# Kernel optimization log

Measured on AMD Instinct MI355X. Metric: run time of the kernel, lower is better.

The kernel has to match this reference:

```python
import jax, jax.numpy as jnp
import numpy as np

NUM_HEADS = 4
LN_EPS = 1e-5
ALPHA_SCALE = 2.0


def setup_inputs() -> dict:
    key = jax.random.key(0)
    ks = jax.random.split(key, 8)
    bs, C, H, W = 64, 256, 56, 56
    T, D = 6, 192
    HW = H * W
    w = lambda k, shape: (jax.random.normal(k, shape, jnp.float32) * 0.02)
    return {
        "features": jax.random.normal(ks[0], (bs, C, H, W), jnp.float32),
        "tokens": jax.random.normal(ks[1], (T, bs, D), jnp.float32),
        # mlp: Linear(HW -> T)
        "mlp_w": w(ks[2], (T, HW)), "mlp_b": jnp.zeros((T,), jnp.float32),
        # q: Linear(D -> C)
        "q_w": w(ks[3], (C, D)), "q_b": jnp.zeros((C,), jnp.float32),
        # alpha: Linear(D -> C)
        "alpha_w": w(ks[4], (C, D)), "alpha_b": jnp.zeros((C,), jnp.float32),
        # proj: Linear(C -> D)
        "proj_w": w(ks[5], (D, C)), "proj_b": jnp.zeros((D,), jnp.float32),
        "ln_g": jnp.ones((D,), jnp.float32), "ln_b": jnp.zeros((D,), jnp.float32),
    }


def reference(features, tokens, mlp_w, mlp_b, q_w, q_b,
              alpha_w, alpha_b, proj_w, proj_b, ln_g, ln_b):
    bs, C, H, W = features.shape
    T, _, D = tokens.shape
    h = NUM_HEADS
    dh = C // h
    HW = H * W
    scale = dh ** -0.5

    f = features.reshape(bs, C, HW)

    # mlp branch: Linear over HW -> [bs, C, T] -> permute to [T, bs, C]
    t_sum = jnp.einsum('bcn,tn->tbc', f, mlp_w) + mlp_b[:, None, None]

    # attn branch: few tokens attend over H*W feature map (k reused as v)
    q = jnp.einsum('tbd,cd->tbc', tokens, q_w) + q_b          # [T, bs, C]
    q = q.reshape(T, bs, h, dh).transpose(1, 2, 0, 3)         # [bs, h, T, dh]
    k = f.reshape(bs, h, dh, HW)                              # [bs, h, dh, HW]
    attn = jnp.einsum('bhtd,bhdn->bhtn', q, k) * scale        # [bs, h, T, HW]
    a = jax.nn.softmax(attn, axis=-1)
    attn_out = jnp.einsum('bhtn,bhdn->bhtd', a, k)            # [bs, h, T, dh]
    t_a = attn_out.transpose(2, 0, 1, 3).reshape(T, bs, C)
    t_sum = t_sum + t_a

    # dynamic gate: h_sigmoid(alpha(tokens)) * 2.0
    alp = jnp.clip(jnp.einsum('tbd,cd->tbc', tokens, alpha_w) + alpha_b + 3.0,
                   0.0, 6.0) / 6.0 * ALPHA_SCALE              # [T, bs, C]
    t_sum = t_sum * alp

    # proj + residual + LayerNorm (post-norm, drop_path rate 0 -> identity)
    t_sum = jnp.einsum('tbc,dc->tbd', t_sum, proj_w) + proj_b  # [T, bs, D]
    tok = tokens + t_sum
    mu = tok.mean(-1, keepdims=True)
    var = ((tok - mu) ** 2).mean(-1, keepdims=True)
    tok = (tok - mu) * jax.lax.rsqrt(var + LN_EPS) * ln_g + ln_b

    return tok, attn.reshape(bs, h, T, H, W)
```

## Files before the change

### kernel.cpp

```cpp
#include <hip/hip_runtime.h>
#include <hip/hip_bf16.h>

constexpr int BS = 64, C = 256, NH = 4, DH = 64, T = 6, D = 192;
constexpr int HW = 3136;
constexpr int NT = 64;
constexpr int S = 7, CPB = 7;
constexpr int PNF = 72;
constexpr int PNS = 68;
constexpr int QP = 72;
constexpr float SCALE = 0.125f;
constexpr float LN_EPS = 1e-5f;

typedef short bf16x8 __attribute__((ext_vector_type(8)));
typedef float f32x4 __attribute__((ext_vector_type(4)));

__device__ inline unsigned short f2bf(float x) {
    union { float f; unsigned u; } v; v.f = x;
    unsigned r = v.u + 0x7FFFu + ((v.u >> 16) & 1u);
    return (unsigned short)(r >> 16);
}

__device__ inline void st_bf8(unsigned short* dst, float4 p) {
    unsigned lo = (unsigned)f2bf(p.x) | ((unsigned)f2bf(p.y) << 16);
    unsigned hi = (unsigned)f2bf(p.z) | ((unsigned)f2bf(p.w) << 16);
    *(uint2*)dst = make_uint2(lo, hi);
}

__device__ inline int fsw(int r, int n) { return n ^ (((r >> 3) & 3) << 4); }

__global__ __launch_bounds__(256) void qalpha_kernel(
    const float* __restrict__ tokens,
    const float* __restrict__ q_w,
    const float* __restrict__ q_b,
    const float* __restrict__ alpha_w,
    const float* __restrict__ alpha_b,
    float* __restrict__ q_ws,
    float* __restrict__ alp_ws)
{
    int b = blockIdx.x;
    int c = threadIdx.x;
    __shared__ float tok_s[T][D];
    for (int i = c; i < T * (D / 4); i += 256) {
        int t = i / (D / 4), v = i % (D / 4);
        *(float4*)&tok_s[t][4 * v] =
            *(const float4*)&tokens[((size_t)t * BS + b) * D + 4 * v];
    }
    __syncthreads();

    const float4* qr = (const float4*)(q_w + (size_t)c * D);
    const float4* ar = (const float4*)(alpha_w + (size_t)c * D);
    float accq[T] = {0, 0, 0, 0, 0, 0};
    float acca[T] = {0, 0, 0, 0, 0, 0};
    for (int v = 0; v < D / 4; ++v) {
        float4 qw4 = qr[v], aw4 = ar[v];
#pragma unroll
        for (int t = 0; t < T; ++t) {
            float4 t4 = *(const float4*)&tok_s[t][4 * v];
            accq[t] += qw4.x * t4.x + qw4.y * t4.y + qw4.z * t4.z + qw4.w * t4.w;
            acca[t] += aw4.x * t4.x + aw4.y * t4.y + aw4.z * t4.z + aw4.w * t4.w;
        }
    }
    float qb = q_b[c], ab = alpha_b[c];
#pragma unroll
    for (int t = 0; t < T; ++t) {
        size_t idx = ((size_t)t * BS + b) * C + c;
        q_ws[idx] = accq[t] + qb;
        float aa = acca[t] + ab + 3.0f;
        alp_ws[idx] = fminf(fmaxf(aa, 0.0f), 6.0f) * (2.0f / 6.0f);
    }
}

__global__ __launch_bounds__(64) void fused_attn_mlp(
    const float* __restrict__ feat,
    const float* __restrict__ mlp_w,
    const float* __restrict__ q_ws,
    float* __restrict__ out_attn,
    float* __restrict__ o_part,
    float* __restrict__ mlp_part,
    float* __restrict__ ml_part)
{
    int bh = blockIdx.x / S, sp = blockIdx.x % S;
    int b = bh / NH, h = bh % NH;
    int lane = threadIdx.x;
    int col = lane & 15, quad = lane >> 4;

    __shared__ unsigned short fch[DH][PNF];
    __shared__ unsigned short pw[16][PNF];
    __shared__ unsigned short qs[16][QP];
    __shared__ float st[T][PNS];
    __shared__ float m_s[8], l_s[8], al_s[16];

    const float* fbase = feat + ((size_t)b * C + h * DH) * HW;
    const float* fl  = fbase + (size_t)quad * HW + 4 * col;
    const float* ml0 = mlp_w + (size_t)quad * HW + 4 * col;
    const float* ml1 = mlp_w + (size_t)(4 + (quad & 1)) * HW + 4 * col;
    float* obase = out_attn + ((size_t)bh * T) * HW;

    float4 pf[16];
    float4 pm0, pm1;

    auto pf_issue = [&](int n0) {
#pragma unroll
        for (int i = 0; i < 16; ++i)
            pf[i] = *(const float4*)&fl[(size_t)(4 * i) * HW + n0];
        pm0 = *(const float4*)&ml0[n0];
        if (lane < 32) pm1 = *(const float4*)&ml1[n0];
    };
    auto pf_commit = [&]() {
#pragma unroll
        for (int i = 0; i < 16; ++i) {
            int r = 4 * i + quad;
            st_bf8(&fch[r][fsw(r, 4 * col)], pf[i]);
        }
        { int rm = 6 + quad; st_bf8(&pw[rm][fsw(rm, 4 * col)], pm0); }
        if (lane < 32) { int rm = 10 + quad; st_bf8(&pw[rm][fsw(rm, 4 * col)], pm1); }
    };

    const int nsp = sp * CPB * NT;
    pf_issue(nsp);

    for (int i = lane; i < 4 * PNF; i += 64) pw[12 + i / PNF][i % PNF] = 0;
    if (lane < T) { m_s[lane] = -3e38f; l_s[lane] = 0.f; }
#pragma unroll
    for (int t = 0; t < T; ++t)
        qs[t][lane] = f2bf(q_ws[((size_t)t * BS + b) * C + h * DH + lane]);
    bf16x8 a0 = *(const bf16x8*)&qs[col][quad * 8];
    bf16x8 a1 = *(const bf16x8*)&qs[col][32 + quad * 8];

    f32x4 acc[4];
#pragma unroll
    for (int ct = 0; ct < 4; ++ct) acc[ct] = (f32x4){0.f, 0.f, 0.f, 0.f};

#pragma unroll 1
    for (int cc = 0; cc < CPB; ++cc) {
        const int n0 = nsp + cc * NT;

        pf_commit();
        if (cc + 1 < CPB) pf_issue(n0 + NT);

#pragma unroll
        for (int tile = 0; tile < 4; ++tile) {
            int nsw = (tile * 16 + col) ^ (quad << 4);
            bf16x8 b0, b1;
#pragma unroll
            for (int j = 0; j < 8; ++j) {
                b0[j] = (short)fch[quad * 8 + j][nsw];
                b1[j] = (short)fch[32 + quad * 8 + j][nsw];
            }
            f32x4 sa = {0.f, 0.f, 0.f, 0.f};
            sa = __builtin_amdgcn_mfma_f32_16x16x32_bf16(a0, b0, sa, 0, 0, 0);
            sa = __builtin_amdgcn_mfma_f32_16x16x32_bf16(a1, b1, sa, 0, 0, 0);
#pragma unroll
            for (int reg = 0; reg < 4; ++reg) {
                int r = quad * 4 + reg;
                if (r < 6) st[r][tile * 16 + col] = sa[reg] * SCALE;
            }
        }

#pragma unroll
        for (int t = 0; t < T; ++t) {
            float v = st[t][lane];
            float mloc = v;
#pragma unroll
            for (int off = 32; off; off >>= 1) mloc = fmaxf(mloc, __shfl_xor(mloc, off));
            float m_old = m_s[t], m_new = fmaxf(m_old, mloc);
            float p = __expf(v - m_new);
            pw[t][lane] = f2bf(p);
            float ssum = p;
#pragma unroll
            for (int off = 32; off; off >>= 1) ssum += __shfl_xor(ssum, off);
            if (lane == 0) {
                float a = __expf(m_old - m_new);
                al_s[t] = a;
                l_s[t] = l_s[t] * a + ssum;
                m_s[t] = m_new;
            }
            if (lane < NT / 4)
                *(float4*)&obase[(size_t)t * HW + n0 + 4 * lane] =
                    *(const float4*)&st[t][4 * lane];
        }

        float alpha = (col < 6) ? al_s[col] : 1.0f;
#pragma unroll
        for (int ct = 0; ct < 4; ++ct) {
            acc[ct] *= alpha;
            int ra = ct * 16 + col;
#pragma unroll
            for (int ks = 0; ks < 2; ++ks) {
                bf16x8 af = *(const bf16x8*)&fch[ra][fsw(ra, ks * 32 + quad * 8)];
                bf16x8 bf = *(const bf16x8*)&pw[col][fsw(col, ks * 32 + quad * 8)];
                acc[ct] = __builtin_amdgcn_mfma_f32_16x16x32_bf16(af, bf, acc[ct], 0, 0, 0);
            }
        }
    }

#pragma unroll
    for (int ct = 0; ct < 4; ++ct) {
#pragma unroll
        for (int reg = 0; reg < 4; ++reg) {
            int c2 = ct * 16 + quad * 4 + reg;
            if (col < 6) {
                o_part[((size_t)blockIdx.x * T + col) * DH + c2] = acc[ct][reg];
            } else if (col < 12) {
                mlp_part[((size_t)blockIdx.x * T + (col - 6)) * DH + c2] = acc[ct][reg];
            }
        }
    }
    if (lane < 2 * T) {
        int t = lane >> 1;
        ml_part[((size_t)blockIdx.x * T + t) * 2 + (lane & 1)] =
            (lane & 1) ? l_s[t] : m_s[t];
    }
}

__global__ __launch_bounds__(256) void merge_proj_ln_kernel(
    const float* __restrict__ o_part,
    const float* __restrict__ mlp_part,
    const float* __restrict__ ml_part,
    const float* __restrict__ mlp_b,
    const float* __restrict__ alp_ws,
    const float* __restrict__ tokens,
    const float* __restrict__ proj_w,
    const float* __restrict__ proj_b,
    const float* __restrict__ ln_g,
    const float* __restrict__ ln_b,
    float* __restrict__ out_tok)
{
    int tb = blockIdx.x;
    int t = tb / BS, b = tb % BS;
    int tid = threadIdx.x;
    __shared__ float g_s[C];
    __shared__ float r1[4], r2[4];

    {
        int c = tid;
        int h = c >> 6, cl = c & 63;
        int bh = b * NH + h;
        float m[S], l[S];
        float M = -3e38f;
#pragma unroll
        for (int s = 0; s < S; ++s) {
            size_t blk = (size_t)(bh * S + s);
            m[s] = ml_part[(blk * T + t) * 2 + 0];
            l[s] = ml_part[(blk * T + t) * 2 + 1];
            M = fmaxf(M, m[s]);
        }
        float L = 0.f, O = 0.f, MLP = 0.f;
#pragma unroll
        for (int s = 0; s < S; ++s) {
            float w = __expf(m[s] - M);
            size_t blk = (size_t)(bh * S + s);
            size_t pidx = (blk * T + t) * DH + cl;
            L += l[s] * w;
            O += o_part[pidx] * w;
            MLP += mlp_part[pidx];
        }
        size_t idx = (size_t)tb * C + c;
        g_s[c] = (MLP + mlp_b[t] + O / L) * alp_ws[idx];
    }
    __syncthreads();

    if (tid < D) {
        int d = tid;
        float acc = proj_b[d] + tokens[(size_t)tb * D + d];
        const float4* pr = (const float4*)(proj_w + (size_t)d * C);
#pragma unroll 8
        for (int v = 0; v < C / 4; ++v) {
            float4 w4 = pr[v];
            float4 g4 = *(const float4*)&g_s[4 * v];
            acc += w4.x * g4.x + w4.y * g4.y + w4.z * g4.z + w4.w * g4.w;
        }

        float s1 = acc, s2 = acc * acc;
#pragma unroll
        for (int off = 32; off; off >>= 1) { s1 += __shfl_down(s1, off); s2 += __shfl_down(s2, off); }
        int wv = d >> 6, lane = d & 63;
        if (lane == 0) { r1[wv] = s1; r2[wv] = s2; }
        __syncthreads();
        float sum1 = r1[0] + r1[1] + r1[2];
        float sum2 = r2[0] + r2[1] + r2[2];
        float mu = sum1 * (1.0f / D);
        float var = sum2 * (1.0f / D) - mu * mu;
        float inv = rsqrtf(var + LN_EPS);
        out_tok[(size_t)tb * D + d] = (acc - mu) * inv * ln_g[d] + ln_b[d];
    } else {
        __syncthreads();
    }
}

extern "C" void kernel_launch(void* const* d_in, const int* in_sizes, int n_in,
                              void* d_out, int out_size, void* d_ws, size_t ws_size,
                              hipStream_t stream) {
    const float* features = (const float*)d_in[0];
    const float* tokens   = (const float*)d_in[1];
    const float* mlp_w    = (const float*)d_in[2];
    const float* mlp_b    = (const float*)d_in[3];
    const float* q_w      = (const float*)d_in[4];
    const float* q_b      = (const float*)d_in[5];
    const float* alpha_w  = (const float*)d_in[6];
    const float* alpha_b  = (const float*)d_in[7];
    const float* proj_w   = (const float*)d_in[8];
    const float* proj_b   = (const float*)d_in[9];
    const float* ln_g     = (const float*)d_in[10];
    const float* ln_b     = (const float*)d_in[11];

    float* out_tok  = (float*)d_out;
    float* out_attn = (float*)d_out + T * BS * D;

    constexpr int NBLK = BS * NH * S;
    float* q_ws     = (float*)d_ws;
    float* alp_ws   = q_ws + T * BS * C;
    float* ml_part  = alp_ws + T * BS * C;
    float* o_part   = ml_part + NBLK * T * 2;
    float* mlp_part = o_part + NBLK * T * DH;

    qalpha_kernel<<<BS, 256, 0, stream>>>(
        tokens, q_w, q_b, alpha_w, alpha_b, q_ws, alp_ws);

    fused_attn_mlp<<<NBLK, 64, 0, stream>>>(
        features, mlp_w, q_ws, out_attn, o_part, mlp_part, ml_part);

    merge_proj_ln_kernel<<<T * BS, 256, 0, stream>>>(
        o_part, mlp_part, ml_part, mlp_b, alp_ws, tokens,
        proj_w, proj_b, ln_g, ln_b, out_tok);
}
```

Baseline: 354.8 us.

## Split spatial axis into 28 single-tile blocks, drop LDS staging and online softmax

The fused attention/MLP kernel now gives each block a single 112-wide spatial tile, using 28 splits instead of 7 splits that each looped over 7 chunks. Feature values are loaded straight from global memory into MFMA operands rather than staged through LDS, and each block computes a plain local softmax instead of an online rescaling loop. Conversion to bf16 now uses the packed v_cvt_pk_bf16_f32 instruction. This gives four times as many blocks to hide latency and removes LDS round-trips and barriers, at the cost of reading the feature tile twice from global memory (the second read is likely served by cache), scalar strided loads, and four times as many partial results for the merge kernel to reduce.

```diff
diff --git a/kernel.cpp b/kernel.cpp
--- a/kernel.cpp
+++ b/kernel.cpp
@@ -3,11 +3,9 @@
 
 constexpr int BS = 64, C = 256, NH = 4, DH = 64, T = 6, D = 192;
 constexpr int HW = 3136;
-constexpr int NT = 64;
-constexpr int S = 7, CPB = 7;
-constexpr int PNF = 72;
-constexpr int PNS = 68;
-constexpr int QP = 72;
+constexpr int NT = 112;
+constexpr int S = 28;
+constexpr int PWP = 136;
 constexpr float SCALE = 0.125f;
 constexpr float LN_EPS = 1e-5f;
 
@@ -20,13 +18,29 @@
     return (unsigned short)(r >> 16);
 }
 
+__device__ inline unsigned cvtpk(float lo, float hi) {
+    unsigned d;
+    asm("v_cvt_pk_bf16_f32 %0, %1, %2" : "=v"(d) : "v"(lo), "v"(hi));
+    return d;
+}
+
+__device__ inline bf16x8 pk8f4(float4 a, float4 b) {
+    union { unsigned u[4]; bf16x8 v8; } r;
+    r.u[0] = cvtpk(a.x, a.y); r.u[1] = cvtpk(a.z, a.w);
+    r.u[2] = cvtpk(b.x, b.y); r.u[3] = cvtpk(b.z, b.w);
+    return r.v8;
+}
+
+__device__ inline bf16x8 pk8(const float* v) {
+    union { unsigned u[4]; bf16x8 v8; } r;
+    r.u[0] = cvtpk(v[0], v[1]); r.u[1] = cvtpk(v[2], v[3]);
+    r.u[2] = cvtpk(v[4], v[5]); r.u[3] = cvtpk(v[6], v[7]);
+    return r.v8;
+}
+
 __device__ inline void st_bf8(unsigned short* dst, float4 p) {
-    unsigned lo = (unsigned)f2bf(p.x) | ((unsigned)f2bf(p.y) << 16);
-    unsigned hi = (unsigned)f2bf(p.z) | ((unsigned)f2bf(p.w) << 16);
-    *(uint2*)dst = make_uint2(lo, hi);
-}
-
-__device__ inline int fsw(int r, int n) { return n ^ (((r >> 3) & 3) << 4); }
+    *(uint2*)dst = make_uint2(cvtpk(p.x, p.y), cvtpk(p.z, p.w));
+}
 
 __global__ __launch_bounds__(256) void qalpha_kernel(
     const float* __restrict__ tokens,
@@ -83,133 +97,106 @@
     int b = bh / NH, h = bh % NH;
     int lane = threadIdx.x;
     int col = lane & 15, quad = lane >> 4;
-
-    __shared__ unsigned short fch[DH][PNF];
-    __shared__ unsigned short pw[16][PNF];
-    __shared__ unsigned short qs[16][QP];
-    __shared__ float st[T][PNS];
-    __shared__ float m_s[8], l_s[8], al_s[16];
+    const int n0 = sp * NT;
+
+    __shared__ unsigned short pw[16][PWP];
 
     const float* fbase = feat + ((size_t)b * C + h * DH) * HW;
-    const float* fl  = fbase + (size_t)quad * HW + 4 * col;
-    const float* ml0 = mlp_w + (size_t)quad * HW + 4 * col;
-    const float* ml1 = mlp_w + (size_t)(4 + (quad & 1)) * HW + 4 * col;
-    float* obase = out_attn + ((size_t)bh * T) * HW;
-
-    float4 pf[16];
-    float4 pm0, pm1;
-
-    auto pf_issue = [&](int n0) {
-#pragma unroll
-        for (int i = 0; i < 16; ++i)
-            pf[i] = *(const float4*)&fl[(size_t)(4 * i) * HW + n0];
-        pm0 = *(const float4*)&ml0[n0];
-        if (lane < 32) pm1 = *(const float4*)&ml1[n0];
-    };
-    auto pf_commit = [&]() {
-#pragma unroll
-        for (int i = 0; i < 16; ++i) {
-            int r = 4 * i + quad;
-            st_bf8(&fch[r][fsw(r, 4 * col)], pf[i]);
-        }
-        { int rm = 6 + quad; st_bf8(&pw[rm][fsw(rm, 4 * col)], pm0); }
-        if (lane < 32) { int rm = 10 + quad; st_bf8(&pw[rm][fsw(rm, 4 * col)], pm1); }
-    };
-
-    const int nsp = sp * CPB * NT;
-    pf_issue(nsp);
-
-    for (int i = lane; i < 4 * PNF; i += 64) pw[12 + i / PNF][i % PNF] = 0;
-    if (lane < T) { m_s[lane] = -3e38f; l_s[lane] = 0.f; }
-#pragma unroll
-    for (int t = 0; t < T; ++t)
-        qs[t][lane] = f2bf(q_ws[((size_t)t * BS + b) * C + h * DH + lane]);
-    bf16x8 a0 = *(const bf16x8*)&qs[col][quad * 8];
-    bf16x8 a1 = *(const bf16x8*)&qs[col][32 + quad * 8];
-
-    f32x4 acc[4];
-#pragma unroll
-    for (int ct = 0; ct < 4; ++ct) acc[ct] = (f32x4){0.f, 0.f, 0.f, 0.f};
-
-#pragma unroll 1
-    for (int cc = 0; cc < CPB; ++cc) {
-        const int n0 = nsp + cc * NT;
-
-        pf_commit();
-        if (cc + 1 < CPB) pf_issue(n0 + NT);
-
-#pragma unroll
-        for (int tile = 0; tile < 4; ++tile) {
-            int nsw = (tile * 16 + col) ^ (quad << 4);
-            bf16x8 b0, b1;
-#pragma unroll
-            for (int j = 0; j < 8; ++j) {
-                b0[j] = (short)fch[quad * 8 + j][nsw];
-                b1[j] = (short)fch[32 + quad * 8 + j][nsw];
+
+    for (int i = lane; i < 4 * PWP; i += 64) pw[12 + i / PWP][i % PWP] = 0;
+    for (int i = lane; i < 12 * 24; i += 64) pw[i / 24][112 + (i % 24)] = 0;
+    for (int i = lane; i < 6 * (NT / 4); i += 64) {
+        int t = i / (NT / 4), v = i % (NT / 4);
+        float4 w4 = *(const float4*)&mlp_w[(size_t)t * HW + n0 + 4 * v];
+        st_bf8(&pw[6 + t][4 * v], w4);
+    }
+
+    int tq = (col < T) ? col : (T - 1);
+    const float* qrow = q_ws + ((size_t)tq * BS + b) * C + h * DH + quad * 8;
+    bf16x8 a0 = pk8f4(*(const float4*)&qrow[0],  *(const float4*)&qrow[4]);
+    bf16x8 a1 = pk8f4(*(const float4*)&qrow[32], *(const float4*)&qrow[36]);
+
+    const float* fcol = fbase + n0 + col;
+    const float* rp[8];
+    const float* rq[8];
+#pragma unroll
+    for (int j = 0; j < 8; ++j) {
+        rp[j] = fcol + (size_t)(quad * 8 + j) * HW;
+        rq[j] = rp[j] + (size_t)32 * HW;
+    }
+
+    f32x4 sc[7];
+#pragma unroll
+    for (int tile = 0; tile < 7; ++tile) {
+        float u[8], w[8];
+#pragma unroll
+        for (int j = 0; j < 8; ++j) { u[j] = rp[j][tile * 16]; w[j] = rq[j][tile * 16]; }
+        f32x4 s = {0.f, 0.f, 0.f, 0.f};
+        s = __builtin_amdgcn_mfma_f32_16x16x32_bf16(a0, pk8(u), s, 0, 0, 0);
+        s = __builtin_amdgcn_mfma_f32_16x16x32_bf16(a1, pk8(w), s, 0, 0, 0);
+        s[0] *= SCALE; s[1] *= SCALE; s[2] *= SCALE; s[3] *= SCALE;
+        sc[tile] = s;
+    }
+
+#pragma unroll
+    for (int r = 0; r < 4; ++r) {
+        int t = quad * 4 + r;
+        if (t < T) {
+            float* dst = out_attn + ((size_t)bh * T + t) * HW + n0 + col;
+#pragma unroll
+            for (int tile = 0; tile < 7; ++tile) dst[tile * 16] = sc[tile][r];
+        }
+    }
+
+#pragma unroll
+    for (int r = 0; r < 4; ++r) {
+        int t = quad * 4 + r;
+        float mx = sc[0][r];
+#pragma unroll
+        for (int tile = 1; tile < 7; ++tile) mx = fmaxf(mx, sc[tile][r]);
+#pragma unroll
+        for (int off = 1; off < 16; off <<= 1) mx = fmaxf(mx, __shfl_xor(mx, off));
+        float sum = 0.f;
+#pragma unroll
+        for (int tile = 0; tile < 7; ++tile) {
+            float p = __expf(sc[tile][r] - mx);
+            sum += p;
+            sc[tile][r] = p;
+        }
+#pragma unroll
+        for (int off = 1; off < 16; off <<= 1) sum += __shfl_xor(sum, off);
+        if (t < T) {
+#pragma unroll
+            for (int tile = 0; tile < 7; ++tile)
+                pw[t][tile * 16 + col] = f2bf(sc[tile][r]);
+            if (col == 0) {
+                ml_part[((size_t)blockIdx.x * T + t) * 2 + 0] = mx;
+                ml_part[((size_t)blockIdx.x * T + t) * 2 + 1] = sum;
             }
-            f32x4 sa = {0.f, 0.f, 0.f, 0.f};
-            sa = __builtin_amdgcn_mfma_f32_16x16x32_bf16(a0, b0, sa, 0, 0, 0);
-            sa = __builtin_amdgcn_mfma_f32_16x16x32_bf16(a1, b1, sa, 0, 0, 0);
-#pragma unroll
-            for (int reg = 0; reg < 4; ++reg) {
-                int r = quad * 4 + reg;
-                if (r < 6) st[r][tile * 16 + col] = sa[reg] * SCALE;
-            }
-        }
-
-#pragma unroll
-        for (int t = 0; t < T; ++t) {
-            float v = st[t][lane];
-            float mloc = v;
-#pragma unroll
-            for (int off = 32; off; off >>= 1) mloc = fmaxf(mloc, __shfl_xor(mloc, off));
-            float m_old = m_s[t], m_new = fmaxf(m_old, mloc);
-            float p = __expf(v - m_new);
-            pw[t][lane] = f2bf(p);
-            float ssum = p;
-#pragma unroll
-            for (int off = 32; off; off >>= 1) ssum += __shfl_xor(ssum, off);
-            if (lane == 0) {
-                float a = __expf(m_old - m_new);
-                al_s[t] = a;
-                l_s[t] = l_s[t] * a + ssum;
-                m_s[t] = m_new;
-            }
-            if (lane < NT / 4)
-                *(float4*)&obase[(size_t)t * HW + n0 + 4 * lane] =
-                    *(const float4*)&st[t][4 * lane];
-        }
-
-        float alpha = (col < 6) ? al_s[col] : 1.0f;
-#pragma unroll
-        for (int ct = 0; ct < 4; ++ct) {
-            acc[ct] *= alpha;
-            int ra = ct * 16 + col;
-#pragma unroll
-            for (int ks = 0; ks < 2; ++ks) {
-                bf16x8 af = *(const bf16x8*)&fch[ra][fsw(ra, ks * 32 + quad * 8)];
-                bf16x8 bf = *(const bf16x8*)&pw[col][fsw(col, ks * 32 + quad * 8)];
-                acc[ct] = __builtin_amdgcn_mfma_f32_16x16x32_bf16(af, bf, acc[ct], 0, 0, 0);
-            }
         }
     }
 
 #pragma unroll
     for (int ct = 0; ct < 4; ++ct) {
+        f32x4 a = {0.f, 0.f, 0.f, 0.f};
+        const float* ar = fbase + (size_t)(ct * 16 + col) * HW;
+#pragma unroll
+        for (int ks = 0; ks < 4; ++ks) {
+            int nn = n0 + ks * 32 + quad * 8;
+            if (nn > HW - 8) nn = HW - 8;
+            bf16x8 af = pk8f4(*(const float4*)&ar[nn], *(const float4*)&ar[nn + 4]);
+            bf16x8 bfp = *(const bf16x8*)&pw[col][ks * 32 + quad * 8];
+            a = __builtin_amdgcn_mfma_f32_16x16x32_bf16(af, bfp, a, 0, 0, 0);
+        }
 #pragma unroll
         for (int reg = 0; reg < 4; ++reg) {
             int c2 = ct * 16 + quad * 4 + reg;
             if (col < 6) {
-                o_part[((size_t)blockIdx.x * T + col) * DH + c2] = acc[ct][reg];
+                o_part[((size_t)blockIdx.x * T + col) * DH + c2] = a[reg];
             } else if (col < 12) {
-                mlp_part[((size_t)blockIdx.x * T + (col - 6)) * DH + c2] = acc[ct][reg];
+                mlp_part[((size_t)blockIdx.x * T + (col - 6)) * DH + c2] = a[reg];
             }
         }
-    }
-    if (lane < 2 * T) {
-        int t = lane >> 1;
-        ml_part[((size_t)blockIdx.x * T + t) * 2 + (lane & 1)] =
-            (lane & 1) ? l_s[t] : m_s[t];
     }
 }
 
@@ -236,22 +223,17 @@
         int c = tid;
         int h = c >> 6, cl = c & 63;
         int bh = b * NH + h;
-        float m[S], l[S];
         float M = -3e38f;
-#pragma unroll
-        for (int s = 0; s < S; ++s) {
-            size_t blk = (size_t)(bh * S + s);
-            m[s] = ml_part[(blk * T + t) * 2 + 0];
-            l[s] = ml_part[(blk * T + t) * 2 + 1];
-            M = fmaxf(M, m[s]);
-        }
+        for (int s2 = 0; s2 < S; ++s2)
+            M = fmaxf(M, ml_part[((size_t)(bh * S + s2) * T + t) * 2 + 0]);
         float L = 0.f, O = 0.f, MLP = 0.f;
-#pragma unroll
-        for (int s = 0; s < S; ++s) {
-            float w = __expf(m[s] - M);
-            size_t blk = (size_t)(bh * S + s);
+        for (int s2 = 0; s2 < S; ++s2) {
+            size_t blk = (size_t)(bh * S + s2);
+            float m = ml_part[(blk * T + t) * 2 + 0];
+            float l = ml_part[(blk * T + t) * 2 + 1];
+            float w = __expf(m - M);
             size_t pidx = (blk * T + t) * DH + cl;
-            L += l[s] * w;
+            L += l * w;
             O += o_part[pidx] * w;
             MLP += mlp_part[pidx];
         }
```

New measurement: 369.2 us. 1.04x slower.
